# Kernel optimization log

Measured on AMD Instinct MI355X. Metric: run time of the kernel, lower is better.

The kernel has to match this reference:

```python
import jax, jax.numpy as jnp
import numpy as np

B, S, D, H, E = 4, 2048, 2048, 4096, 8
TOP_K = 2
ENTROPY_WEIGHT = 0.1
MAX_USAGE_RATIO = 0.3


def setup_inputs() -> dict:
    key = jax.random.key(0)
    k0, k1, k2 = jax.random.split(key, 3)
    x = jax.random.normal(k0, (B, S, D), dtype=jnp.float32)
    gate_w = jax.random.normal(k1, (E, D), dtype=jnp.float32) * 0.02
    gate_b = jnp.zeros((E,), dtype=jnp.float32)
    expert_w = jax.random.normal(k2, (E, H, D), dtype=jnp.float32) * 0.02
    expert_b = jnp.zeros((E, H), dtype=jnp.float32)
    return {"x": x, "gate_w": gate_w, "gate_b": gate_b,
            "expert_w": expert_w, "expert_b": expert_b}


def reference(x, gate_w, gate_b, expert_w, expert_b):
    b, s, d = x.shape
    e, h, _ = expert_w.shape
    n = b * s
    xf = x.reshape(n, d)

    # gating
    gate_logits = xf @ gate_w.T + gate_b              # (N, E)
    gate_probs = jax.nn.softmax(gate_logits, axis=-1)
    entropy = (-jnp.sum(gate_probs * jnp.log(gate_probs + 1e-10), axis=-1)).mean()
    entropy_loss = ENTROPY_WEIGHT * entropy

    # top-k dispatch weights
    topk_probs, topk_idx = jax.lax.top_k(gate_probs, TOP_K)   # (N, K)
    combine = jnp.sum(jax.nn.one_hot(topk_idx, e, dtype=xf.dtype)
                      * topk_probs[..., None], axis=1)        # (N, E)

    # per-expert linear + weighted combine (loop over small fixed E)
    out = jnp.zeros((n, h), dtype=xf.dtype)
    for ei in range(e):
        out = out + combine[:, ei:ei + 1] * (xf @ expert_w[ei].T + expert_b[ei])

    # usage penalty (this batch's routing counts)
    counts = jnp.sum(jax.nn.one_hot(topk_idx, e, dtype=jnp.float32), axis=(0, 1))
    usage_ratios = counts / n
    overuse_penalty = jnp.sum(jax.nn.relu(usage_ratios - MAX_USAGE_RATIO))

    return out.reshape(b, s, h), entropy_loss + overuse_penalty
```

## Files before the change

kernel.cpp:

```cpp
#include <hip/hip_runtime.h>

constexpr int N_TOK = 8192;
constexpr int D_IN  = 2048;
constexpr int H_OUT = 4096;
constexpr int NEXP  = 8;
constexpr float ENT_W = 0.1f;
constexpr float MAX_USAGE = 0.3f;

constexpr int TM = 128;
constexpr int TH = 128;
constexpr int BK = 32;
constexpr int NKT = D_IN / BK;
constexpr int TILES_H = H_OUT / TH;
constexpr int TM_MAX  = N_TOK / TM;
constexpr int REGION  = 8192;
constexpr int BUFSZ   = TM * BK;

typedef __attribute__((ext_vector_type(8))) short bf16x8;
typedef __attribute__((ext_vector_type(4))) float f32x4;

__device__ __forceinline__ short f2bf(float f) {
    unsigned u = __float_as_uint(f);
    u += 0x7FFF + ((u >> 16) & 1);
    return (short)(u >> 16);
}

__device__ __forceinline__ void gload16(const void* g, void* l) {
    __builtin_amdgcn_global_load_lds(
        (const __attribute__((address_space(1))) unsigned int*)g,
        (__attribute__((address_space(3))) unsigned int*)l, 16, 0, 0);
}

__global__ __launch_bounds__(256) void cvt_kernel(
    const float* __restrict__ in, short* __restrict__ out, int n8)
{
    int stride = gridDim.x * 256;
    for (int i = blockIdx.x * 256 + threadIdx.x; i < n8; i += stride) {
        const float4* p = (const float4*)in + (size_t)i * 2;
        float4 a = p[0], b = p[1];
        bf16x8 v;
        v[0] = f2bf(a.x); v[1] = f2bf(a.y); v[2] = f2bf(a.z); v[3] = f2bf(a.w);
        v[4] = f2bf(b.x); v[5] = f2bf(b.y); v[6] = f2bf(b.z); v[7] = f2bf(b.w);
        *(bf16x8*)(out + (size_t)i * 8) = v;
    }
}

__global__ __launch_bounds__(256) void gate_kernel(
    const float* __restrict__ x, const float* __restrict__ gate_w,
    const float* __restrict__ gate_b, int* __restrict__ topk_idx,
    float* __restrict__ topk_w, float* __restrict__ ent_partial,
    short* __restrict__ xb)
{
    __shared__ float ent_s[4];
    const int wv = threadIdx.x >> 6;
    const int lane = threadIdx.x & 63;
    const int t = blockIdx.x * 4 + wv;

    float acc[NEXP];
#pragma unroll
    for (int e = 0; e < NEXP; ++e) acc[e] = 0.f;

    const float4* xr = (const float4*)(x + (size_t)t * D_IN);
    short* xbr = xb + (size_t)t * D_IN;
#pragma unroll
    for (int i = 0; i < D_IN / 256; ++i) {
        float4 xv = xr[lane + i * 64];
        short4 s4;
        s4.x = f2bf(xv.x); s4.y = f2bf(xv.y); s4.z = f2bf(xv.z); s4.w = f2bf(xv.w);
        *(short4*)(xbr + i * 256 + lane * 4) = s4;
#pragma unroll
        for (int e = 0; e < NEXP; ++e) {
            float4 gv = ((const float4*)(gate_w + e * D_IN))[lane + i * 64];
            acc[e] += xv.x * gv.x + xv.y * gv.y + xv.z * gv.z + xv.w * gv.w;
        }
    }
#pragma unroll
    for (int e = 0; e < NEXP; ++e)
#pragma unroll
        for (int m = 32; m >= 1; m >>= 1) acc[e] += __shfl_xor(acc[e], m, 64);

    if (lane == 0) {
        float lg[NEXP], p[NEXP];
        float mx = -1e30f;
#pragma unroll
        for (int e = 0; e < NEXP; ++e) { lg[e] = acc[e] + gate_b[e]; mx = fmaxf(mx, lg[e]); }
        float s = 0.f;
#pragma unroll
        for (int e = 0; e < NEXP; ++e) { p[e] = expf(lg[e] - mx); s += p[e]; }
        float inv = 1.f / s;
        float ent = 0.f;
#pragma unroll
        for (int e = 0; e < NEXP; ++e) { p[e] *= inv; ent -= p[e] * logf(p[e] + 1e-10f); }
        int e1 = 0; float b1 = p[0];
#pragma unroll
        for (int e = 1; e < NEXP; ++e) if (p[e] > b1) { b1 = p[e]; e1 = e; }
        int e2 = (e1 == 0) ? 1 : 0; float b2 = p[e2];
#pragma unroll
        for (int e = 0; e < NEXP; ++e)
            if (e != e1 && e != ((e1 == 0) ? 1 : 0) && p[e] > b2) { b2 = p[e]; e2 = e; }
        topk_idx[2 * t]     = e1;  topk_idx[2 * t + 1] = e2;
        topk_w[2 * t]       = b1;  topk_w[2 * t + 1]   = b2;
        ent_s[wv] = ent;
    }
    __syncthreads();
    if (threadIdx.x == 0)
        ent_partial[blockIdx.x] = ent_s[0] + ent_s[1] + ent_s[2] + ent_s[3];
}

__global__ __launch_bounds__(256) void scatter_kernel(
    const int* __restrict__ topk_idx, const float* __restrict__ topk_w,
    int* __restrict__ cursors, int* __restrict__ tok_list,
    float* __restrict__ w_list)
{
    __shared__ int lcnt[NEXP], lbase[NEXP];
    const int tid = threadIdx.x;
    const int t = blockIdx.x * 256 + tid;
    if (tid < NEXP) lcnt[tid] = 0;
    __syncthreads();
    int e0 = topk_idx[2 * t], e1 = topk_idx[2 * t + 1];
    float w0 = topk_w[2 * t], w1 = topk_w[2 * t + 1];
    int p0 = atomicAdd(&lcnt[e0], 1);
    int p1 = atomicAdd(&lcnt[e1], 1);
    __syncthreads();
    if (tid < NEXP) lbase[tid] = atomicAdd(&cursors[tid], lcnt[tid]);
    __syncthreads();
    int d0 = e0 * REGION + lbase[e0] + p0;
    int d1 = e1 * REGION + lbase[e1] + p1;
    tok_list[d0] = t;  w_list[d0] = w0;
    tok_list[d1] = t;  w_list[d1] = w1;
}

__global__ __launch_bounds__(256) void finalize_kernel(
    const int* __restrict__ counts, const float* __restrict__ ent_partial,
    float* __restrict__ loss_out)
{
    __shared__ float red[256];
    float s = 0.f;
    for (int i = threadIdx.x; i < N_TOK / 4; i += 256) s += ent_partial[i];
    red[threadIdx.x] = s;
    __syncthreads();
    for (int st = 128; st > 0; st >>= 1) {
        if (threadIdx.x < st) red[threadIdx.x] += red[threadIdx.x + st];
        __syncthreads();
    }
    if (threadIdx.x == 0) {
        float loss = ENT_W * red[0] / (float)N_TOK;
        for (int e = 0; e < NEXP; ++e) {
            float r = (float)counts[e] / (float)N_TOK - MAX_USAGE;
            if (r > 0.f) loss += r;
        }
        loss_out[0] = loss;
    }
}

__global__ __launch_bounds__(256, 3) void moe_gemm(
    const short* __restrict__ xb, const short* __restrict__ wb,
    const float* __restrict__ expert_b, const int* __restrict__ tok_list,
    const float* __restrict__ w_list, const int* __restrict__ counts,
    float* __restrict__ out)
{
    const int bid = blockIdx.x;
    const int e   = bid / (TM_MAX * TILES_H);
    const int rem = bid % (TM_MAX * TILES_H);
    const int tm  = rem / TILES_H;
    const int th  = rem % TILES_H;

    const int cnt = counts[e];
    if (tm * TM >= cnt) return;
    const int valid = cnt - tm * TM;
    const int hbase = th * TH;

    __shared__ __align__(16) short A_s[3][BUFSZ];
    __shared__ __align__(16) short B_s[3][BUFSZ];
    __shared__ int   tok_s[TM];
    __shared__ float wgt_s[TM];

    const int tid = threadIdx.x;
    if (tid < TM) {
        bool v = tid < valid;
        int src = e * REGION + tm * TM + tid;
        tok_s[tid] = v ? tok_list[src] : 0;
        wgt_s[tid] = v ? w_list[src] : 0.f;
    }
    __syncthreads();

    const int lane = tid & 63;
    const int wv = tid >> 6;

    const char* asrc[2];
    const char* bsrc[2];
    int dst_off[2];
#pragma unroll
    for (int j = 0; j < 2; ++j) {
        int c = wv * 2 + j;
        int r = c * 16 + (lane >> 2);
        int s2 = (lane & 3) ^ ((lane >> 3) & 3);
        asrc[j] = (const char*)(xb + (size_t)tok_s[r] * D_IN) + s2 * 16;
        bsrc[j] = (const char*)(wb + ((size_t)e * H_OUT + hbase + r) * D_IN) + s2 * 16;
        dst_off[j] = c * 512;
    }

    const int rr = lane & 15, kg = lane >> 4;
    const int wr = wv >> 1, wc = wv & 1;

    int aoff[4], boff[4];
#pragma unroll
    for (int mi = 0; mi < 4; ++mi) {
        int row = wr * 64 + mi * 16 + rr;
        aoff[mi] = row * 32 + (kg ^ ((row >> 1) & 3)) * 8;
        int rowb = wc * 64 + mi * 16 + rr;
        boff[mi] = rowb * 32 + (kg ^ ((rowb >> 1) & 3)) * 8;
    }

    f32x4 acc[4][4] = {};

#define STAGE_KT(slot)                                                     \
    {                                                                      \
        short* Aso = (short*)A_s[slot];                                    \
        short* Bso = (short*)B_s[slot];                                    \
        gload16(asrc[0], Aso + dst_off[0]); asrc[0] += BK * 2;             \
        gload16(bsrc[0], Bso + dst_off[0]); bsrc[0] += BK * 2;             \
        gload16(asrc[1], Aso + dst_off[1]); asrc[1] += BK * 2;             \
        gload16(bsrc[1], Bso + dst_off[1]); bsrc[1] += BK * 2;             \
    }

    STAGE_KT(0);
    STAGE_KT(1);
    asm volatile("s_waitcnt vmcnt(4)" ::: "memory");
    __builtin_amdgcn_sched_barrier(0);
    __builtin_amdgcn_s_barrier();

    for (int kt = 0; kt < NKT; ++kt) {
        const int slot = kt % 3;
        const int nslot = (kt + 2) % 3;
        const short* Ac = A_s[slot];
        const short* Bc = B_s[slot];
        const bool pre = (kt + 2 < NKT);

        if (pre) STAGE_KT(nslot);

        bf16x8 af[4], bv[4];
#pragma unroll
        for (int mi = 0; mi < 4; ++mi) af[mi] = *(const bf16x8*)&Ac[aoff[mi]];
#pragma unroll
        for (int ni = 0; ni < 4; ++ni) bv[ni] = *(const bf16x8*)&Bc[boff[ni]];
        asm volatile("s_waitcnt lgkmcnt(0)" ::: "memory");
        __builtin_amdgcn_sched_barrier(0);

        __builtin_amdgcn_s_setprio(1);
#pragma unroll
        for (int mi = 0; mi < 4; ++mi)
#pragma unroll
            for (int ni = 0; ni < 4; ++ni)
                acc[mi][ni] = __builtin_amdgcn_mfma_f32_16x16x32_bf16(
                    af[mi], bv[ni], acc[mi][ni], 0, 0, 0);
        __builtin_amdgcn_s_setprio(0);

        if (pre) {
            asm volatile("s_waitcnt vmcnt(4)" ::: "memory");
        } else if (kt + 1 < NKT) {
            asm volatile("s_waitcnt vmcnt(0)" ::: "memory");
        }
        __builtin_amdgcn_sched_barrier(0);
        __builtin_amdgcn_s_barrier();
    }
#undef STAGE_KT

    const float* bias = expert_b + (size_t)e * H_OUT + hbase;
#pragma unroll
    for (int mi = 0; mi < 4; ++mi) {
#pragma unroll
        for (int ni = 0; ni < 4; ++ni) {
            int col = wc * 64 + ni * 16 + rr;
            float be = bias[col];
#pragma unroll
            for (int i = 0; i < 4; ++i) {
                int r = wr * 64 + mi * 16 + kg * 4 + i;
                if (r < valid) {
                    float val = wgt_s[r] * (acc[mi][ni][i] + be);
                    atomicAdd(&out[(size_t)tok_s[r] * H_OUT + hbase + col], val);
                }
            }
        }
    }
}

extern "C" void kernel_launch(void* const* d_in, const int* in_sizes, int n_in,
                              void* d_out, int out_size, void* d_ws, size_t ws_size,
                              hipStream_t stream) {
    const float* x        = (const float*)d_in[0];
    const float* gate_w   = (const float*)d_in[1];
    const float* gate_b   = (const float*)d_in[2];
    const float* expert_w = (const float*)d_in[3];
    const float* expert_b = (const float*)d_in[4];
    float* out = (float*)d_out;
    char* ws = (char*)d_ws;

    int*   topk_idx    = (int*)(ws);
    float* topk_w      = (float*)(ws + (64 << 10));
    int*   cursors     = (int*)(ws + (128 << 10));
    float* ent_partial = (float*)(ws + (128 << 10) + 256);
    int*   tok_list    = (int*)(ws + (160 << 10));
    float* w_list      = (float*)(ws + (416 << 10));
    short* xb          = (short*)(ws + (1ull << 20));
    short* wb          = (short*)(ws + (34ull << 20));

    hipMemsetAsync(cursors, 0, 64, stream);
    hipMemsetAsync(d_out, 0, (size_t)out_size * sizeof(float), stream);

    gate_kernel<<<N_TOK / 4, 256, 0, stream>>>(x, gate_w, gate_b, topk_idx,
                                               topk_w, ent_partial, xb);
    cvt_kernel<<<4096, 256, 0, stream>>>(expert_w, wb, (NEXP * H_OUT * D_IN) / 8);
    scatter_kernel<<<N_TOK / 256, 256, 0, stream>>>(topk_idx, topk_w, cursors,
                                                    tok_list, w_list);
    finalize_kernel<<<1, 256, 0, stream>>>(cursors, ent_partial,
                                           out + (size_t)N_TOK * H_OUT);
    moe_gemm<<<NEXP * TM_MAX * TILES_H, 256, 0, stream>>>(
        xb, wb, expert_b, tok_list, w_list, cursors, out);
}
```

Baseline: 704.1 us.

## Fuse weight conversion into gate kernel, double-buffer GEMM and raise occupancy

After: 1.715 ms. 144% more time.

```diff
diff --git a/kernel.cpp b/kernel.cpp
--- a/kernel.cpp
+++ b/kernel.cpp
@@ -31,25 +31,12 @@
         (__attribute__((address_space(3))) unsigned int*)l, 16, 0, 0);
 }
 
-__global__ __launch_bounds__(256) void cvt_kernel(
-    const float* __restrict__ in, short* __restrict__ out, int n8)
-{
-    int stride = gridDim.x * 256;
-    for (int i = blockIdx.x * 256 + threadIdx.x; i < n8; i += stride) {
-        const float4* p = (const float4*)in + (size_t)i * 2;
-        float4 a = p[0], b = p[1];
-        bf16x8 v;
-        v[0] = f2bf(a.x); v[1] = f2bf(a.y); v[2] = f2bf(a.z); v[3] = f2bf(a.w);
-        v[4] = f2bf(b.x); v[5] = f2bf(b.y); v[6] = f2bf(b.z); v[7] = f2bf(b.w);
-        *(bf16x8*)(out + (size_t)i * 8) = v;
-    }
-}
-
-__global__ __launch_bounds__(256) void gate_kernel(
+__global__ __launch_bounds__(256) void gate_cvt_kernel(
     const float* __restrict__ x, const float* __restrict__ gate_w,
     const float* __restrict__ gate_b, int* __restrict__ topk_idx,
     float* __restrict__ topk_w, float* __restrict__ ent_partial,
-    short* __restrict__ xb)
+    short* __restrict__ xb,
+    const float* __restrict__ expert_w, short* __restrict__ wb)
 {
     __shared__ float ent_s[4];
     const int wv = threadIdx.x >> 6;
@@ -105,6 +92,17 @@
     __syncthreads();
     if (threadIdx.x == 0)
         ent_partial[blockIdx.x] = ent_s[0] + ent_s[1] + ent_s[2] + ent_s[3];
+
+    const int n8 = (NEXP * H_OUT * D_IN) / 8;
+    int stride = gridDim.x * 256;
+    for (int i = blockIdx.x * 256 + threadIdx.x; i < n8; i += stride) {
+        const float4* p = (const float4*)expert_w + (size_t)i * 2;
+        float4 a = p[0], b = p[1];
+        bf16x8 v;
+        v[0] = f2bf(a.x); v[1] = f2bf(a.y); v[2] = f2bf(a.z); v[3] = f2bf(a.w);
+        v[4] = f2bf(b.x); v[5] = f2bf(b.y); v[6] = f2bf(b.z); v[7] = f2bf(b.w);
+        *(bf16x8*)(wb + (size_t)i * 8) = v;
+    }
 }
 
 __global__ __launch_bounds__(256) void scatter_kernel(
@@ -153,7 +151,7 @@
     }
 }
 
-__global__ __launch_bounds__(256, 3) void moe_gemm(
+__global__ __launch_bounds__(256, 5) void moe_gemm(
     const short* __restrict__ xb, const short* __restrict__ wb,
     const float* __restrict__ expert_b, const int* __restrict__ tok_list,
     const float* __restrict__ w_list, const int* __restrict__ counts,
@@ -168,22 +166,13 @@
     const int cnt = counts[e];
     if (tm * TM >= cnt) return;
     const int valid = cnt - tm * TM;
+    const int base  = e * REGION + tm * TM;
     const int hbase = th * TH;
 
-    __shared__ __align__(16) short A_s[3][BUFSZ];
-    __shared__ __align__(16) short B_s[3][BUFSZ];
-    __shared__ int   tok_s[TM];
-    __shared__ float wgt_s[TM];
+    __shared__ __align__(16) short A_s[2][BUFSZ];
+    __shared__ __align__(16) short B_s[2][BUFSZ];
 
     const int tid = threadIdx.x;
-    if (tid < TM) {
-        bool v = tid < valid;
-        int src = e * REGION + tm * TM + tid;
-        tok_s[tid] = v ? tok_list[src] : 0;
-        wgt_s[tid] = v ? w_list[src] : 0.f;
-    }
-    __syncthreads();
-
     const int lane = tid & 63;
     const int wv = tid >> 6;
 
@@ -195,7 +184,8 @@
         int c = wv * 2 + j;
         int r = c * 16 + (lane >> 2);
         int s2 = (lane & 3) ^ ((lane >> 3) & 3);
-        asrc[j] = (const char*)(xb + (size_t)tok_s[r] * D_IN) + s2 * 16;
+        int tok = (r < valid) ? tok_list[base + r] : tok_list[base];
+        asrc[j] = (const char*)(xb + (size_t)tok * D_IN) + s2 * 16;
         bsrc[j] = (const char*)(wb + ((size_t)e * H_OUT + hbase + r) * D_IN) + s2 * 16;
         dst_off[j] = c * 512;
     }
@@ -214,10 +204,10 @@
 
     f32x4 acc[4][4] = {};
 
-#define STAGE_KT(slot)                                                     \
+#define STAGE_KT(buf)                                                      \
     {                                                                      \
-        short* Aso = (short*)A_s[slot];                                    \
-        short* Bso = (short*)B_s[slot];                                    \
+        short* Aso = (short*)A_s[buf];                                     \
+        short* Bso = (short*)B_s[buf];                                     \
         gload16(asrc[0], Aso + dst_off[0]); asrc[0] += BK * 2;             \
         gload16(bsrc[0], Bso + dst_off[0]); bsrc[0] += BK * 2;             \
         gload16(asrc[1], Aso + dst_off[1]); asrc[1] += BK * 2;             \
@@ -231,13 +221,8 @@
     __builtin_amdgcn_s_barrier();
 
     for (int kt = 0; kt < NKT; ++kt) {
-        const int slot = kt % 3;
-        const int nslot = (kt + 2) % 3;
-        const short* Ac = A_s[slot];
-        const short* Bc = B_s[slot];
-        const bool pre = (kt + 2 < NKT);
-
-        if (pre) STAGE_KT(nslot);
+        const short* Ac = A_s[kt & 1];
+        const short* Bc = B_s[kt & 1];
 
         bf16x8 af[4], bv[4];
 #pragma unroll
@@ -246,6 +231,9 @@
         for (int ni = 0; ni < 4; ++ni) bv[ni] = *(const bf16x8*)&Bc[boff[ni]];
         asm volatile("s_waitcnt lgkmcnt(0)" ::: "memory");
         __builtin_amdgcn_sched_barrier(0);
+        __builtin_amdgcn_s_barrier();
+
+        if (kt + 2 < NKT) STAGE_KT(kt & 1);
 
         __builtin_amdgcn_s_setprio(1);
 #pragma unroll
@@ -256,7 +244,7 @@
                     af[mi], bv[ni], acc[mi][ni], 0, 0, 0);
         __builtin_amdgcn_s_setprio(0);
 
-        if (pre) {
+        if (kt + 2 < NKT) {
             asm volatile("s_waitcnt vmcnt(4)" ::: "memory");
         } else if (kt + 1 < NKT) {
             asm volatile("s_waitcnt vmcnt(0)" ::: "memory");
@@ -267,18 +255,22 @@
 #undef STAGE_KT
 
     const float* bias = expert_b + (size_t)e * H_OUT + hbase;
+    float be[4];
+#pragma unroll
+    for (int ni = 0; ni < 4; ++ni) be[ni] = bias[wc * 64 + ni * 16 + rr];
 #pragma unroll
     for (int mi = 0; mi < 4; ++mi) {
 #pragma unroll
-        for (int ni = 0; ni < 4; ++ni) {
-            int col = wc * 64 + ni * 16 + rr;
-            float be = bias[col];
-#pragma unroll
-            for (int i = 0; i < 4; ++i) {
-                int r = wr * 64 + mi * 16 + kg * 4 + i;
-                if (r < valid) {
-                    float val = wgt_s[r] * (acc[mi][ni][i] + be);
-                    atomicAdd(&out[(size_t)tok_s[r] * H_OUT + hbase + col], val);
+        for (int i = 0; i < 4; ++i) {
+            int r = wr * 64 + mi * 16 + kg * 4 + i;
+            if (r < valid) {
+                int tok  = tok_list[base + r];
+                float w  = w_list[base + r];
+                float* orow = out + (size_t)tok * H_OUT + hbase;
+#pragma unroll
+                for (int ni = 0; ni < 4; ++ni) {
+                    int col = wc * 64 + ni * 16 + rr;
+                    atomicAdd(orow + col, w * (acc[mi][ni][i] + be[ni]));
                 }
             }
         }
@@ -308,13 +300,13 @@
     hipMemsetAsync(cursors, 0, 64, stream);
     hipMemsetAsync(d_out, 0, (size_t)out_size * sizeof(float), stream);
 
-    gate_kernel<<<N_TOK / 4, 256, 0, stream>>>(x, gate_w, gate_b, topk_idx,
-                                               topk_w, ent_partial, xb);
-    cvt_kernel<<<4096, 256, 0, stream>>>(expert_w, wb, (NEXP * H_OUT * D_IN) / 8);
+    gate_cvt_kernel<<<N_TOK / 4, 256, 0, stream>>>(x, gate_w, gate_b, topk_idx,
+                                                   topk_w, ent_partial, xb,
+                                                   expert_w, wb);
     scatter_kernel<<<N_TOK / 256, 256, 0, stream>>>(topk_idx, topk_w, cursors,
                                                     tok_list, w_list);
+    moe_gemm<<<NEXP * TM_MAX * TILES_H, 256, 0, stream>>>(
+        xb, wb, expert_b, tok_list, w_list, cursors, out);
     finalize_kernel<<<1, 256, 0, stream>>>(cursors, ent_partial,
                                            out + (size_t)N_TOK * H_OUT);
-    moe_gemm<<<NEXP * TM_MAX * TILES_H, 256, 0, stream>>>(
-        xb, wb, expert_b, tok_list, w_list, cursors, out);
-}
+}
```
